# Kernel tuning notes

Measured on AMD Instinct MI355X. Metric: run time of the kernel, lower is better.

## Reference

```python
import jax, jax.numpy as jnp
import numpy as np
from jax import lax

TAU = 2.0
NUM_HEADS = 8
EPS = 1e-5
ALPHA = 4.0  # surrogate sigmoid sharpness

@jax.custom_vjp
def heaviside(x):
    # torch.heaviside(x, 1.0): 1 for x >= 0 (value 1 at x==0), 0 for x < 0
    return (x >= 0).astype(x.dtype)

def _hv_fwd(x):
    return (x >= 0).astype(x.dtype), x

def _hv_bwd(x, g):
    s = jax.nn.sigmoid(x * ALPHA)
    return (g * s * (1.0 - s) * ALPHA,)

heaviside.defvjp(_hv_fwd, _hv_bwd)

def lif(x):
    # Leaky-integrate-fire recurrence over leading time axis. x: [T, ...]
    def step(v, xt):
        v = v + (xt - v) / TAU                 # leakage
        s = heaviside(v - 1.0)                 # fire (v_threshold = 1.0)
        v = (1.0 - lax.stop_gradient(s)) * v   # hard reset (detached spike)
        return v, s
    _, spikes = lax.scan(step, jnp.zeros_like(x[0]), x)
    return spikes

def conv1x1(x, w):
    # x: [T,B,Cin,H,W], w: [Cout,Cin] (1x1 conv, no bias)
    return jnp.einsum('tbchw,dc->tbdhw', x, w)

def bn(x, gamma, beta, mean, var):
    # BatchNorm2d in eval mode (running stats), per-channel over axis 2
    shp = (1, 1, -1, 1, 1)
    inv = gamma.reshape(shp) / jnp.sqrt(var.reshape(shp) + EPS)
    return (x - mean.reshape(shp)) * inv + beta.reshape(shp)

def setup_inputs():
    key = jax.random.key(0)
    ks = jax.random.split(key, 10)
    T, B, C, H, W = 4, 32, 256, 16, 16
    Cv = C  # lamda_ratio = 1

    def w_init(k, o, i):
        return jax.random.normal(k, (o, i), jnp.float32) * (1.0 / np.sqrt(i))

    def bn_params(k, c):
        k1, k2, k3, k4 = jax.random.split(k, 4)
        gamma = jax.random.uniform(k1, (c,), jnp.float32, 0.5, 1.5)
        beta = jax.random.normal(k2, (c,), jnp.float32) * 0.1
        mean = jax.random.normal(k3, (c,), jnp.float32) * 0.1
        var = jax.random.uniform(k4, (c,), jnp.float32, 0.5, 1.5)
        return gamma, beta, mean, var

    x = jax.random.normal(ks[0], (T, B, C, H, W), jnp.float32)
    q_w = w_init(ks[1], C, C)
    k_w = w_init(ks[2], C, C)
    v_w = w_init(ks[3], Cv, C)
    proj_w = w_init(ks[4], C, Cv)
    q_gamma, q_beta, q_mean, q_var = bn_params(ks[5], C)
    k_gamma, k_beta, k_mean, k_var = bn_params(ks[6], C)
    v_gamma, v_beta, v_mean, v_var = bn_params(ks[7], Cv)
    p_gamma, p_beta, p_mean, p_var = bn_params(ks[8], C)
    return {
        'x': x,
        'q_w': q_w, 'q_gamma': q_gamma, 'q_beta': q_beta, 'q_mean': q_mean, 'q_var': q_var,
        'k_w': k_w, 'k_gamma': k_gamma, 'k_beta': k_beta, 'k_mean': k_mean, 'k_var': k_var,
        'v_w': v_w, 'v_gamma': v_gamma, 'v_beta': v_beta, 'v_mean': v_mean, 'v_var': v_var,
        'proj_w': proj_w, 'p_gamma': p_gamma, 'p_beta': p_beta, 'p_mean': p_mean, 'p_var': p_var,
    }

def reference(x, q_w, q_gamma, q_beta, q_mean, q_var,
              k_w, k_gamma, k_beta, k_mean, k_var,
              v_w, v_gamma, v_beta, v_mean, v_var,
              proj_w, p_gamma, p_beta, p_mean, p_var):
    T, B, C, H, W = x.shape
    N = H * W
    Cv = v_w.shape[0]
    hd = C // NUM_HEADS
    hdv = Cv // NUM_HEADS
    scale = (C // NUM_HEADS) ** -0.5

    xs = lif(x)  # head_spike

    q = lif(bn(conv1x1(xs, q_w), q_gamma, q_beta, q_mean, q_var))  # [T,B,C,H,W] binary
    k = lif(bn(conv1x1(xs, k_w), k_gamma, k_beta, k_mean, k_var))
    v = lif(bn(conv1x1(xs, v_w), v_gamma, v_beta, v_mean, v_var))  # [T,B,Cv,H,W]

    # channel c = h*hd + d; flatten spatial -> tokens N, split heads
    q = q.reshape(T, B, NUM_HEADS, hd, N).transpose(0, 1, 2, 4, 3)   # [T,B,h,N,d]
    k = k.reshape(T, B, NUM_HEADS, hd, N).transpose(0, 1, 2, 4, 3)
    v = v.reshape(T, B, NUM_HEADS, hdv, N).transpose(0, 1, 2, 4, 3)  # [T,B,h,N,dv]

    attn = jnp.einsum('tbhnd,tbhmd->tbhnm', q, k)                    # QK^T
    out = jnp.einsum('tbhnm,tbhmd->tbhnd', attn, v) * (scale * 2.0)  # (QK^T)V * 2*scale

    out = out.transpose(0, 1, 2, 4, 3).reshape(T, B, Cv, N)          # [T,B,Cv,N]
    out = lif(out)                                                   # attn_spike
    out = out.reshape(T, B, Cv, H, W)
    out = bn(conv1x1(out, proj_w), p_gamma, p_beta, p_mean, p_var)   # [T,B,C,H,W]
    return out
```

## Files before the change

kernel.cpp:

```cpp
#include <hip/hip_runtime.h>

#define TT 4
#define BB 32
#define CC 256
#define NN 256
#define EPSf 1e-5f
#define MULTf 0.35355339059327373f
#define MARGINf 1e-3f
#define FLAG_CAP 524288u

typedef __attribute__((ext_vector_type(8))) short s16x8;
typedef __attribute__((ext_vector_type(4))) float f32x4;
typedef unsigned char uchar;
typedef unsigned int uint;
typedef unsigned short ushort;

__device__ __forceinline__ ushort f2bf_rn(float f) {
  uint u = __float_as_uint(f);
  u = (u + 0x7FFFu + ((u >> 16) & 1u)) >> 16;
  return (ushort)u;
}
__device__ __forceinline__ float bf2f(ushort b) {
  return __uint_as_float(((uint)b) << 16);
}

__device__ __forceinline__ void gload_lds16(const void* g, void* l) {
  __builtin_amdgcn_global_load_lds(
      (const __attribute__((address_space(1))) uint*)g,
      (__attribute__((address_space(3))) uint*)l, 16, 0, 0);
}

__global__ __launch_bounds__(256) void k_front(
    const float* __restrict__ x, uchar* __restrict__ xsF, uchar* __restrict__ xsP,
    const float* __restrict__ qw, const float* __restrict__ kw,
    const float* __restrict__ vw, const float* __restrict__ pw,
    uchar* __restrict__ wfq, uchar* __restrict__ wfp, uint* __restrict__ flags) {
  const int tid = threadIdx.x;
  const int bid = blockIdx.x;
  if (bid < 1024) {
#pragma clang fp contract(off)
    const int nt = bid & 3;
    const int ks = (bid >> 2) & 7;
    const int b = bid >> 5;
    const int nl = tid & 63;
    const int oct = tid >> 6;
    const int n = nt * 64 + nl;
    const int c0 = ks * 32 + oct * 8;
    const size_t stride = (size_t)BB * CC * NN;
    const float* xb = x + ((size_t)b * CC + c0) * NN + n;

    float v[8];
#pragma unroll
    for (int j = 0; j < 8; ++j) v[j] = 0.f;

#pragma unroll
    for (int t = 0; t < TT; ++t) {
      ushort sp[8];
      uint pm = 0;
#pragma unroll
      for (int j = 0; j < 8; ++j) {
        float xt = xb[t * stride + (size_t)j * NN];
        float d = (xt - v[j]) * 0.5f;
        v[j] = v[j] + d;
        bool s = (v[j] >= 1.0f);
        sp[j] = s ? (ushort)0x3F80 : (ushort)0;
        if (s) { v[j] = 0.f; pm |= 1u << j; }
      }
      uint4* dst = reinterpret_cast<uint4*>(xsF) +
                   (((size_t)(t * BB + b) * 16 + (n >> 4)) * 512 + ks * 64 + oct * 16 + (n & 15));
      uint4 o;
      o.x = (uint)sp[0] | ((uint)sp[1] << 16);
      o.y = (uint)sp[2] | ((uint)sp[3] << 16);
      o.z = (uint)sp[4] | ((uint)sp[5] << 16);
      o.w = (uint)sp[6] | ((uint)sp[7] << 16);
      *dst = o;
      xsP[(((size_t)(t * BB + b) * NN + n) << 5) + ks * 4 + oct] = (uchar)pm;
    }
  } else {
    const int gid = (bid - 1024) * 256 + tid;
    if (gid < 4) flags[gid] = 0;
    const int ob2 = gid >> 9;
    const int e = gid & 511;
    const int ks = e >> 6, l = e & 63;
    const float* W;
    uchar* outb;
    int ob_out, nob;
    if (ob2 < 48) {
      const int sel = ob2 >> 4;
      W = sel == 0 ? qw : (sel == 1 ? kw : vw);
      W += ((size_t)((ob2 & 15) * 16 + (l & 15))) * CC;
      outb = wfq; ob_out = ob2; nob = 48;
    } else {
      W = pw + ((size_t)((ob2 - 48) * 16 + (l & 15))) * CC;
      outb = wfp; ob_out = ob2 - 48; nob = 16;
    }
    const int c0 = ks * 32 + (l >> 4) * 8;
    float wv[8];
    *reinterpret_cast<float4*>(&wv[0]) = *reinterpret_cast<const float4*>(W + c0);
    *reinterpret_cast<float4*>(&wv[4]) = *reinterpret_cast<const float4*>(W + c0 + 4);
    ushort hi[8], lo[8];
#pragma unroll
    for (int j = 0; j < 8; ++j) {
      hi[j] = f2bf_rn(wv[j]);
      lo[j] = f2bf_rn(wv[j] - bf2f(hi[j]));
    }
    const size_t base = (((size_t)ob_out * 8 + ks) * 64 + l) * 16;
    const size_t sstr = (size_t)nob * 8 * 64 * 16;
    *reinterpret_cast<uint4*>(outb + base) = *reinterpret_cast<const uint4*>(hi);
    *reinterpret_cast<uint4*>(outb + sstr + base) = *reinterpret_cast<const uint4*>(lo);
  }
}

__global__ __launch_bounds__(256) void k_qkv_mfma(
    const uchar* __restrict__ xsF, const uchar* __restrict__ wfq,
    const float* __restrict__ qga, const float* __restrict__ qbe, const float* __restrict__ qme, const float* __restrict__ qva,
    const float* __restrict__ kga, const float* __restrict__ kbe, const float* __restrict__ kme, const float* __restrict__ kva,
    const float* __restrict__ vga, const float* __restrict__ vbe, const float* __restrict__ vme, const float* __restrict__ vva,
    ushort* __restrict__ qp, uint* __restrict__ flags) {
  __shared__ short wlds[64][64][8];
  const int tid = threadIdx.x;
  const int w = tid >> 6, lane = tid & 63;
  const int lhi = lane >> 4, llo = lane & 15;
  const int wr = w >> 1, wc = w & 1;
  const int bid = blockIdx.x;
  const int xcd = bid & 7;
  const int r = bid >> 3;
  const int j = r % 12;
  const int g = (r / 12) * 8 + xcd;
  const int b = g >> 2, ntile = g & 3;
  const int oc0 = j * 64;
  const int sel = j >> 2;
  const float* G  = sel == 0 ? qga : (sel == 1 ? kga : vga);
  const float* Be = sel == 0 ? qbe : (sel == 1 ? kbe : vbe);
  const float* Mn = sel == 0 ? qme : (sel == 1 ? kme : vme);
  const float* Vr = sel == 0 ? qva : (sel == 1 ? kva : vva);

#pragma unroll
  for (int i = 0; i < 16; ++i) {
    const int cg = w * 16 + i;
    const int s = cg >> 5, rem = cg & 31, obl = rem >> 3, ks = rem & 7;
    const size_t gsrc = ((((size_t)s * 48 + j * 4 + obl) * 8 + ks) * 64 + lane) * 16;
    gload_lds16(wfq + gsrc, reinterpret_cast<char*>(&wlds[0][0][0]) + cg * 1024);
  }

  float inv8[2][4], mean8[2][4], beta8[2][4];
#pragma unroll
  for (int mf = 0; mf < 2; ++mf)
#pragma unroll
    for (int rr = 0; rr < 4; ++rr) {
      const int ocb = (oc0 & 255) + wr * 32 + mf * 16 + lhi * 4 + rr;
      inv8[mf][rr] = G[ocb] / sqrtf(Vr[ocb] + EPSf);
      mean8[mf][rr] = Mn[ocb];
      beta8[mf][rr] = Be[ocb];
    }

  float vst[2][2][4];
#pragma unroll
  for (int mf = 0; mf < 2; ++mf)
#pragma unroll
    for (int nf = 0; nf < 2; ++nf)
#pragma unroll
      for (int rr = 0; rr < 4; ++rr) vst[mf][nf][rr] = 0.f;
  uint fl = 0;
  ushort qm[TT][4];

  const int nb0 = ntile * 4 + wc * 2;
  __syncthreads();

#define BPTR(t_, nb_, ks_)                                              \
  reinterpret_cast<const s16x8*>(                                       \
      xsF + ((((size_t)((t_) * BB + b) * 16 + (nb_)) * 512 + (ks_) * 64 + lane) * 16))

  s16x8 bA[2][8], bB[2][8];
#pragma unroll
  for (int ks = 0; ks < 8; ++ks) {
    bA[0][ks] = *BPTR(0, nb0, ks);
    bA[1][ks] = *BPTR(0, nb0 + 1, ks);
  }

#define QKV_STEP(t_, CUR, NXT, PRE)                                             \
  {                                                                             \
    if (PRE) {                                                                  \
      _Pragma("unroll") for (int ks = 0; ks < 8; ++ks) {                        \
        NXT[0][ks] = *BPTR((t_) + 1, nb0, ks);                                  \
        NXT[1][ks] = *BPTR((t_) + 1, nb0 + 1, ks);                              \
      }                                                                         \
    }                                                                           \
    f32x4 acc[2][2];                                                            \
    _Pragma("unroll") for (int mf = 0; mf < 2; ++mf)                            \
        _Pragma("unroll") for (int nf = 0; nf < 2; ++nf)                        \
            acc[mf][nf] = (f32x4){0.f, 0.f, 0.f, 0.f};                          \
    _Pragma("unroll") for (int ks = 0; ks < 8; ++ks) {                          \
      _Pragma("unroll") for (int s = 0; s < 2; ++s)                             \
          _Pragma("unroll") for (int mf = 0; mf < 2; ++mf) {                    \
        s16x8 wf = *reinterpret_cast<const s16x8*>(                             \
            &wlds[s * 32 + (wr * 2 + mf) * 8 + ks][lane][0]);                   \
        acc[mf][0] = __builtin_amdgcn_mfma_f32_16x16x32_bf16(wf, CUR[0][ks],    \
                                                             acc[mf][0], 0, 0, 0); \
        acc[mf][1] = __builtin_amdgcn_mfma_f32_16x16x32_bf16(wf, CUR[1][ks],    \
                                                             acc[mf][1], 0, 0, 0); \
      }                                                                         \
    }                                                                           \
    _Pragma("unroll") for (int mf = 0; mf < 2; ++mf)                            \
        _Pragma("unroll") for (int nf = 0; nf < 2; ++nf)                        \
            _Pragma("unroll") for (int rr = 0; rr < 4; ++rr) {                  \
      float y = (acc[mf][nf][rr] - mean8[mf][rr]) * inv8[mf][rr] + beta8[mf][rr]; \
      float v = vst[mf][nf][rr];                                                \
      v = v + (y - v) * 0.5f;                                                   \
      const bool sp = (v >= 1.0f);                                              \
      if (fabsf(v - 1.0f) < MARGINf) fl |= 1u << ((mf * 2 + nf) * 4 + rr);      \
      const unsigned long long m = __ballot(sp);                                \
      if (llo == rr) qm[t_][mf * 2 + nf] = (ushort)((m >> (lhi * 16)) & 0xFFFFull); \
      vst[mf][nf][rr] = sp ? 0.f : v;                                           \
    }                                                                           \
  }

  QKV_STEP(0, bA, bB, 1)
  QKV_STEP(1, bB, bA, 1)
  QKV_STEP(2, bA, bB, 1)
  QKV_STEP(3, bB, bA, 0)
#undef QKV_STEP
#undef BPTR

  if (llo < 4) {
#pragma unroll
    for (int t = 0; t < TT; ++t) {
      ushort* qrow = qp + (size_t)(t * BB + b) * 768 * 16;
#pragma unroll
      for (int mf = 0; mf < 2; ++mf)
#pragma unroll
        for (int nf = 0; nf < 2; ++nf) {
          const int oc = oc0 + wr * 32 + mf * 16 + lhi * 4 + llo;
          qrow[(size_t)oc * 16 + ntile * 4 + wc * 2 + nf] = qm[t][mf * 2 + nf];
        }
    }
  }

  if (fl) {
    const int cnt = __popc(fl);
    uint base = atomicAdd(flags, (uint)cnt);
#pragma unroll
    for (int mf = 0; mf < 2; ++mf)
#pragma unroll
      for (int nf = 0; nf < 2; ++nf)
#pragma unroll
        for (int rr = 0; rr < 4; ++rr)
          if (fl & (1u << ((mf * 2 + nf) * 4 + rr))) {
            const int oc = oc0 + wr * 32 + mf * 16 + lhi * 4 + rr;
            const int n = ntile * 64 + wc * 32 + nf * 16 + llo;
            if (base < FLAG_CAP) flags[4 + base] = (((uint)(b << 10) | (uint)oc) << 8) | (uint)n;
            base++;
          }
  }
}

__global__ __launch_bounds__(256) void k_fix(
    const uchar* __restrict__ xsP,
    const float* __restrict__ qw, const float* __restrict__ kw, const float* __restrict__ vw,
    const float* __restrict__ qga, const float* __restrict__ qbe, const float* __restrict__ qme, const float* __restrict__ qva,
    const float* __restrict__ kga, const float* __restrict__ kbe, const float* __restrict__ kme, const float* __restrict__ kva,
    const float* __restrict__ vga, const float* __restrict__ vbe, const float* __restrict__ vme, const float* __restrict__ vva,
    uint* __restrict__ qp32, const uint* __restrict__ flags) {
#pragma clang fp contract(off)
  const uint cnt = min(flags[0], FLAG_CAP);
  for (uint i = blockIdx.x * 256 + threadIdx.x; i < cnt; i += gridDim.x * 256) {
    const uint e = flags[4 + i];
    const int n = e & 255;
    const int oc = (e >> 8) & 1023;
    const int b = e >> 18;
    const int sel = oc >> 8, ocl = oc & 255;
    const float* W = (sel == 0 ? qw : (sel == 1 ? kw : vw)) + (size_t)ocl * CC;
    const float* G  = sel == 0 ? qga : (sel == 1 ? kga : vga);
    const float* Be = sel == 0 ? qbe : (sel == 1 ? kbe : vbe);
    const float* Mn = sel == 0 ? qme : (sel == 1 ? kme : vme);
    const float* Vr = sel == 0 ? qva : (sel == 1 ? kva : vva);

    uint bw[4][8];
#pragma unroll
    for (int t = 0; t < TT; ++t) {
      const uint4* p = reinterpret_cast<const uint4*>(
          xsP + (((size_t)(t * BB + b) * NN + n) << 5));
      uint4 a = p[0], c4 = p[1];
      bw[t][0] = a.x;  bw[t][1] = a.y;  bw[t][2] = a.z;  bw[t][3] = a.w;
      bw[t][4] = c4.x; bw[t][5] = c4.y; bw[t][6] = c4.z; bw[t][7] = c4.w;
    }

    const float4* W4 = reinterpret_cast<const float4*>(W);
    float a0 = 0.f, a1 = 0.f, a2 = 0.f, a3 = 0.f;
#pragma unroll
    for (int g = 0; g < 32; ++g) {
      const float4 w0 = W4[2 * g];
      const float4 w1 = W4[2 * g + 1];
      const uint s0 = bw[0][g >> 2] >> ((g & 3) * 8);
      const uint s1 = bw[1][g >> 2] >> ((g & 3) * 8);
      const uint s2 = bw[2][g >> 2] >> ((g & 3) * 8);
      const uint s3 = bw[3][g >> 2] >> ((g & 3) * 8);
      const float wv[8] = {w0.x, w0.y, w0.z, w0.w, w1.x, w1.y, w1.z, w1.w};
#pragma unroll
      for (int jj = 0; jj < 8; ++jj) {
        a0 = fmaf(wv[jj], (float)((s0 >> jj) & 1u), a0);
        a1 = fmaf(wv[jj], (float)((s1 >> jj) & 1u), a1);
        a2 = fmaf(wv[jj], (float)((s2 >> jj) & 1u), a2);
        a3 = fmaf(wv[jj], (float)((s3 >> jj) & 1u), a3);
      }
    }
    float accs[4] = {a0, a1, a2, a3};

    const float inv = G[ocl] / sqrtf(Vr[ocl] + EPSf);
    const float mean = Mn[ocl], beta = Be[ocl];
    float v = 0.f;
#pragma unroll
    for (int t = 0; t < TT; ++t) {
      float xm = accs[t] - mean;
      float y = xm * inv;
      y = y + beta;
      float d = (y - v) * 0.5f;
      v = v + d;
      const bool sp = (v >= 1.0f);
      const size_t widx = ((size_t)(t * BB + b) * 768 + oc) * 8 + (n >> 5);
      const uint bit = 1u << (n & 31);
      if (sp) atomicOr(&qp32[widx], bit);
      else atomicAnd(&qp32[widx], ~bit);
      if (sp) v = 0.f;
    }
  }
}

__global__ __launch_bounds__(1024) void k_attn(const ushort* __restrict__ qp,
                                               uchar* __restrict__ attnF) {
  __shared__ uint Qb[32][8], Kb[32][8], Vb[32][8];
  __shared__ int KtV[32][32];
  const int tid = threadIdx.x;
  const int b = blockIdx.x >> 3;
  const int h = blockIdx.x & 7;
  const int n = tid & 255;
  const int jg = tid >> 8;
  const int wordn = n >> 5, bitn = n & 31;

  float vst[8];
#pragma unroll
  for (int j = 0; j < 8; ++j) vst[j] = 0.f;

  for (int t = 0; t < TT; ++t) {
    __syncthreads();
    const ushort* base = qp + (size_t)(t * BB + b) * 768 * 16;
    if (tid < 768) {
      const int arr = tid >> 8;
      const int idx = tid & 255;
      const int ch = idx >> 3, wv2 = idx & 7;
      const uint val = *reinterpret_cast<const uint*>(
          base + (size_t)(arr * 256 + h * 32 + ch) * 16 + wv2 * 2);
      uint(*dst)[8] = (arr == 0) ? Qb : (arr == 1) ? Kb : Vb;
      dst[ch][wv2] = val;
    }
    __syncthreads();
    {
      const int ii = tid >> 5, jj = tid & 31;
      int s = 0;
#pragma unroll
      for (int w8 = 0; w8 < 8; ++w8) s += __popc(Kb[ii][w8] & Vb[jj][w8]);
      KtV[ii][jj] = s;
    }
    __syncthreads();
    int acc[8];
#pragma unroll
    for (int j = 0; j < 8; ++j) acc[j] = 0;
#pragma unroll 4
    for (int ii = 0; ii < 32; ++ii) {
      const int qb = (int)((Qb[ii][wordn] >> bitn) & 1u);
      const int4 k0 = *reinterpret_cast<const int4*>(&KtV[ii][jg * 8]);
      const int4 k1 = *reinterpret_cast<const int4*>(&KtV[ii][jg * 8 + 4]);
      acc[0] += k0.x * qb; acc[1] += k0.y * qb;
      acc[2] += k0.z * qb; acc[3] += k0.w * qb;
      acc[4] += k1.x * qb; acc[5] += k1.y * qb;
      acc[6] += k1.z * qb; acc[7] += k1.w * qb;
    }
    ushort sbit[8];
    {
#pragma clang fp contract(off)
#pragma unroll
      for (int j = 0; j < 8; ++j) {
        float y = (float)acc[j] * MULTf;
        float v = vst[j];
        float d = (y - v) * 0.5f;
        v = v + d;
        const bool sp = (v >= 1.0f);
        sbit[j] = sp ? (ushort)0x3F80 : (ushort)0;
        vst[j] = sp ? 0.f : v;
      }
    }
    uint4 o;
    o.x = (uint)sbit[0] | ((uint)sbit[1] << 16);
    o.y = (uint)sbit[2] | ((uint)sbit[3] << 16);
    o.z = (uint)sbit[4] | ((uint)sbit[5] << 16);
    o.w = (uint)sbit[6] | ((uint)sbit[7] << 16);
    uint4* dst4 = reinterpret_cast<uint4*>(attnF) +
                  (((size_t)(t * BB + b) * 16 + (n >> 4)) * 512 + h * 64 + jg * 16 + (n & 15));
    *dst4 = o;
  }
}

__global__ __launch_bounds__(256) void k_proj_mfma(
    const uchar* __restrict__ attnF, const uchar* __restrict__ wfp,
    const float* __restrict__ pga, const float* __restrict__ pbe,
    const float* __restrict__ pme, const float* __restrict__ pva,
    float* __restrict__ out) {
  const int tid = threadIdx.x;
  const int w = tid >> 6, lane = tid & 63;
  const int lhi = lane >> 4, llo = lane & 15;
  const int wr = w >> 1, wc = w & 1;
  const int bid = blockIdx.x;
  const int xcd = bid & 7;
  const int r = bid >> 3;
  const int j = r & 3;
  const int g = (r >> 2) * 8 + xcd;
  const int tb = g >> 2, ntile = g & 3;
  const int oc0 = j * 64;

  s16x8 wfr[2][2][8];
#pragma unroll
  for (int s = 0; s < 2; ++s)
#pragma unroll
    for (int mf = 0; mf < 2; ++mf) {
      const int ob = j * 4 + wr * 2 + mf;
#pragma unroll
      for (int ks = 0; ks < 8; ++ks)
        wfr[s][mf][ks] = *reinterpret_cast<const s16x8*>(
            wfp + ((((size_t)s * 16 + ob) * 8 + ks) * 64 + lane) * 16);
    }

  const int nb0 = ntile * 4 + wc * 2;
  s16x8 bfr[2][8];
#pragma unroll
  for (int ks = 0; ks < 8; ++ks) {
    bfr[0][ks] = *reinterpret_cast<const s16x8*>(
        attnF + ((((size_t)tb * 16 + nb0) * 512 + ks * 64 + lane) * 16));
    bfr[1][ks] = *reinterpret_cast<const s16x8*>(
        attnF + ((((size_t)tb * 16 + nb0 + 1) * 512 + ks * 64 + lane) * 16));
  }

  float inv8[2][4], mean8[2][4], beta8[2][4];
#pragma unroll
  for (int mf = 0; mf < 2; ++mf)
#pragma unroll
    for (int rr = 0; rr < 4; ++rr) {
      const int ocb = oc0 + wr * 32 + mf * 16 + lhi * 4 + rr;
      inv8[mf][rr] = pga[ocb] / sqrtf(pva[ocb] + EPSf);
      mean8[mf][rr] = pme[ocb];
      beta8[mf][rr] = pbe[ocb];
    }

  f32x4 acc[2][2];
#pragma unroll
  for (int mf = 0; mf < 2; ++mf)
#pragma unroll
    for (int nf = 0; nf < 2; ++nf) acc[mf][nf] = (f32x4){0.f, 0.f, 0.f, 0.f};

#pragma unroll
  for (int ks = 0; ks < 8; ++ks) {
#pragma unroll
    for (int s = 0; s < 2; ++s)
#pragma unroll
      for (int mf = 0; mf < 2; ++mf) {
        acc[mf][0] = __builtin_amdgcn_mfma_f32_16x16x32_bf16(wfr[s][mf][ks], bfr[0][ks], acc[mf][0], 0, 0, 0);
        acc[mf][1] = __builtin_amdgcn_mfma_f32_16x16x32_bf16(wfr[s][mf][ks], bfr[1][ks], acc[mf][1], 0, 0, 0);
      }
  }

#pragma unroll
  for (int mf = 0; mf < 2; ++mf)
#pragma unroll
    for (int nf = 0; nf < 2; ++nf)
#pragma unroll
      for (int rr = 0; rr < 4; ++rr) {
        const int oc = oc0 + wr * 32 + mf * 16 + lhi * 4 + rr;
        const int nn = ntile * 64 + wc * 32 + nf * 16 + llo;
        float y = (acc[mf][nf][rr] - mean8[mf][rr]) * inv8[mf][rr] + beta8[mf][rr];
        out[((size_t)tb * CC + oc) * NN + nn] = y;
      }
}

extern "C" void kernel_launch(void* const* d_in, const int* in_sizes, int n_in,
                              void* d_out, int out_size, void* d_ws, size_t ws_size,
                              hipStream_t stream) {
  const float* x = (const float*)d_in[0];
  const float* q_w = (const float*)d_in[1];
  const float* q_g = (const float*)d_in[2];
  const float* q_b = (const float*)d_in[3];
  const float* q_m = (const float*)d_in[4];
  const float* q_v = (const float*)d_in[5];
  const float* k_w = (const float*)d_in[6];
  const float* k_g = (const float*)d_in[7];
  const float* k_b = (const float*)d_in[8];
  const float* k_m = (const float*)d_in[9];
  const float* k_v = (const float*)d_in[10];
  const float* v_w = (const float*)d_in[11];
  const float* v_g = (const float*)d_in[12];
  const float* v_b = (const float*)d_in[13];
  const float* v_m = (const float*)d_in[14];
  const float* v_v = (const float*)d_in[15];
  const float* p_w = (const float*)d_in[16];
  const float* p_g = (const float*)d_in[17];
  const float* p_b = (const float*)d_in[18];
  const float* p_m = (const float*)d_in[19];
  const float* p_v = (const float*)d_in[20];

  uchar* ws = (uchar*)d_ws;
  uchar* xsF  = ws;
  ushort* qp  = (ushort*)(ws + 16777216);
  uchar* wfq  = ws + 19922944;
  uchar* wfp  = ws + 20709376;
  uint* flags = (uint*)(ws + 20971520);
  uchar* xsP  = ws + 23068672;

  k_front<<<dim3(1152), 256, 0, stream>>>(x, xsF, xsP, q_w, k_w, v_w, p_w,
                                          wfq, wfp, flags);
  k_qkv_mfma<<<dim3(1536), 256, 0, stream>>>(xsF, wfq,
                                             q_g, q_b, q_m, q_v,
                                             k_g, k_b, k_m, k_v,
                                             v_g, v_b, v_m, v_v,
                                             qp, flags);
  k_fix<<<dim3(64), 256, 0, stream>>>(xsP, q_w, k_w, v_w,
                                      q_g, q_b, q_m, q_v,
                                      k_g, k_b, k_m, k_v,
                                      v_g, v_b, v_m, v_v,
                                      (uint*)qp, flags);
  k_attn<<<dim3(256), 1024, 0, stream>>>(qp, xsF );
  k_proj_mfma<<<dim3(2048), 256, 0, stream>>>(xsF, wfp, p_g, p_b, p_m, p_v,
                                              (float*)d_out);
}
```

Before: 112.3 us.

## Fold BN scale into single-bf16 QKV weights and widen fix-up margin

The QKV weights are now pre-scaled by the BN inverse std and stored as a single bf16 (hi only) instead of a hi/lo split. This halves the MFMA count, and the QKV kernel keeps weight fragments in registers instead of LDS, with one wave per 16-column tile. To absorb the larger bf16 error, the near-threshold margin grows tenfold, the flag capacity grows, and the exact fp32 fix-up kernel launches with more blocks. The front kernel also vectorizes the input LIF to four tokens per thread. The trade is fewer MFMAs and less LDS traffic against possibly many more flagged elements to recompute exactly.

New measurement: 111.0 us. No clear change (-1.2%).

```diff
diff --git a/kernel.cpp b/kernel.cpp
--- a/kernel.cpp
+++ b/kernel.cpp
@@ -6,8 +6,8 @@
 #define NN 256
 #define EPSf 1e-5f
 #define MULTf 0.35355339059327373f
-#define MARGINf 1e-3f
-#define FLAG_CAP 524288u
+#define MARGINQ 1e-2f
+#define FLAG_CAP 2097152u
 
 typedef __attribute__((ext_vector_type(8))) short s16x8;
 typedef __attribute__((ext_vector_type(4))) float f32x4;
@@ -24,109 +24,121 @@
   return __uint_as_float(((uint)b) << 16);
 }
 
-__device__ __forceinline__ void gload_lds16(const void* g, void* l) {
-  __builtin_amdgcn_global_load_lds(
-      (const __attribute__((address_space(1))) uint*)g,
-      (__attribute__((address_space(3))) uint*)l, 16, 0, 0);
-}
-
 __global__ __launch_bounds__(256) void k_front(
     const float* __restrict__ x, uchar* __restrict__ xsF, uchar* __restrict__ xsP,
     const float* __restrict__ qw, const float* __restrict__ kw,
     const float* __restrict__ vw, const float* __restrict__ pw,
+    const float* __restrict__ qga, const float* __restrict__ qva,
+    const float* __restrict__ kga, const float* __restrict__ kva,
+    const float* __restrict__ vga, const float* __restrict__ vva,
     uchar* __restrict__ wfq, uchar* __restrict__ wfp, uint* __restrict__ flags) {
   const int tid = threadIdx.x;
   const int bid = blockIdx.x;
-  if (bid < 1024) {
+  if (bid < 256) {
 #pragma clang fp contract(off)
-    const int nt = bid & 3;
-    const int ks = (bid >> 2) & 7;
-    const int b = bid >> 5;
-    const int nl = tid & 63;
+    const int b = bid >> 3;
+    const int ksq = bid & 7;
     const int oct = tid >> 6;
-    const int n = nt * 64 + nl;
-    const int c0 = ks * 32 + oct * 8;
+    const int nq = tid & 63;
+    const int c0 = ksq * 32 + oct * 8;
+    const int n0 = nq * 4;
     const size_t stride = (size_t)BB * CC * NN;
-    const float* xb = x + ((size_t)b * CC + c0) * NN + n;
-
-    float v[8];
-#pragma unroll
-    for (int j = 0; j < 8; ++j) v[j] = 0.f;
+    const float* xb = x + ((size_t)b * CC + c0) * NN + n0;
+
+    float v[8][4];
+#pragma unroll
+    for (int j = 0; j < 8; ++j)
+#pragma unroll
+      for (int nn = 0; nn < 4; ++nn) v[j][nn] = 0.f;
 
 #pragma unroll
     for (int t = 0; t < TT; ++t) {
-      ushort sp[8];
-      uint pm = 0;
+      ushort sp[8][4];
+      uint pm[4] = {0, 0, 0, 0};
 #pragma unroll
       for (int j = 0; j < 8; ++j) {
-        float xt = xb[t * stride + (size_t)j * NN];
-        float d = (xt - v[j]) * 0.5f;
-        v[j] = v[j] + d;
-        bool s = (v[j] >= 1.0f);
-        sp[j] = s ? (ushort)0x3F80 : (ushort)0;
-        if (s) { v[j] = 0.f; pm |= 1u << j; }
-      }
-      uint4* dst = reinterpret_cast<uint4*>(xsF) +
-                   (((size_t)(t * BB + b) * 16 + (n >> 4)) * 512 + ks * 64 + oct * 16 + (n & 15));
-      uint4 o;
-      o.x = (uint)sp[0] | ((uint)sp[1] << 16);
-      o.y = (uint)sp[2] | ((uint)sp[3] << 16);
-      o.z = (uint)sp[4] | ((uint)sp[5] << 16);
-      o.w = (uint)sp[6] | ((uint)sp[7] << 16);
-      *dst = o;
-      xsP[(((size_t)(t * BB + b) * NN + n) << 5) + ks * 4 + oct] = (uchar)pm;
+        const float4 xv = *reinterpret_cast<const float4*>(xb + t * stride + (size_t)j * NN);
+        const float xa[4] = {xv.x, xv.y, xv.z, xv.w};
+#pragma unroll
+        for (int nn = 0; nn < 4; ++nn) {
+          float d = (xa[nn] - v[j][nn]) * 0.5f;
+          v[j][nn] = v[j][nn] + d;
+          bool s = (v[j][nn] >= 1.0f);
+          sp[j][nn] = s ? (ushort)0x3F80 : (ushort)0;
+          if (s) { v[j][nn] = 0.f; pm[nn] |= 1u << j; }
+        }
+      }
+#pragma unroll
+      for (int nn = 0; nn < 4; ++nn) {
+        const int n = n0 + nn;
+        uint4* dst = reinterpret_cast<uint4*>(xsF) +
+                     (((size_t)(t * BB + b) * 16 + (n >> 4)) * 512 + ksq * 64 + oct * 16 + (n & 15));
+        uint4 o;
+        o.x = (uint)sp[0][nn] | ((uint)sp[1][nn] << 16);
+        o.y = (uint)sp[2][nn] | ((uint)sp[3][nn] << 16);
+        o.z = (uint)sp[4][nn] | ((uint)sp[5][nn] << 16);
+        o.w = (uint)sp[6][nn] | ((uint)sp[7][nn] << 16);
+        *dst = o;
+        xsP[(((size_t)(t * BB + b) * NN + n) << 5) + ksq * 4 + oct] = (uchar)pm[nn];
+      }
     }
   } else {
-    const int gid = (bid - 1024) * 256 + tid;
+    const int gid = (bid - 256) * 256 + tid;
     if (gid < 4) flags[gid] = 0;
     const int ob2 = gid >> 9;
     const int e = gid & 511;
     const int ks = e >> 6, l = e & 63;
-    const float* W;
-    uchar* outb;
-    int ob_out, nob;
+    const int c0 = ks * 32 + (l >> 4) * 8;
     if (ob2 < 48) {
       const int sel = ob2 >> 4;
-      W = sel == 0 ? qw : (sel == 1 ? kw : vw);
-      W += ((size_t)((ob2 & 15) * 16 + (l & 15))) * CC;
-      outb = wfq; ob_out = ob2; nob = 48;
+      const float* Wb = sel == 0 ? qw : (sel == 1 ? kw : vw);
+      const float* G = sel == 0 ? qga : (sel == 1 ? kga : vga);
+      const float* Vr = sel == 0 ? qva : (sel == 1 ? kva : vva);
+      const int ocr = (ob2 & 15) * 16 + (l & 15);
+      const float inv = G[ocr] / sqrtf(Vr[ocr] + EPSf);
+      const float* W = Wb + (size_t)ocr * CC;
+      float wv[8];
+      *reinterpret_cast<float4*>(&wv[0]) = *reinterpret_cast<const float4*>(W + c0);
+      *reinterpret_cast<float4*>(&wv[4]) = *reinterpret_cast<const float4*>(W + c0 + 4);
+      ushort hi[8];
+#pragma unroll
+      for (int j = 0; j < 8; ++j) hi[j] = f2bf_rn(wv[j] * inv);
+      *reinterpret_cast<uint4*>(wfq + (((size_t)ob2 * 8 + ks) * 64 + l) * 16) =
+          *reinterpret_cast<const uint4*>(hi);
     } else {
-      W = pw + ((size_t)((ob2 - 48) * 16 + (l & 15))) * CC;
-      outb = wfp; ob_out = ob2 - 48; nob = 16;
-    }
-    const int c0 = ks * 32 + (l >> 4) * 8;
-    float wv[8];
-    *reinterpret_cast<float4*>(&wv[0]) = *reinterpret_cast<const float4*>(W + c0);
-    *reinterpret_cast<float4*>(&wv[4]) = *reinterpret_cast<const float4*>(W + c0 + 4);
-    ushort hi[8], lo[8];
-#pragma unroll
-    for (int j = 0; j < 8; ++j) {
-      hi[j] = f2bf_rn(wv[j]);
-      lo[j] = f2bf_rn(wv[j] - bf2f(hi[j]));
-    }
-    const size_t base = (((size_t)ob_out * 8 + ks) * 64 + l) * 16;
-    const size_t sstr = (size_t)nob * 8 * 64 * 16;
-    *reinterpret_cast<uint4*>(outb + base) = *reinterpret_cast<const uint4*>(hi);
-    *reinterpret_cast<uint4*>(outb + sstr + base) = *reinterpret_cast<const uint4*>(lo);
-  }
-}
-
-__global__ __launch_bounds__(256) void k_qkv_mfma(
+      const int ob = ob2 - 48;
+      const float* W = pw + ((size_t)(ob * 16 + (l & 15))) * CC;
+      float wv[8];
+      *reinterpret_cast<float4*>(&wv[0]) = *reinterpret_cast<const float4*>(W + c0);
+      *reinterpret_cast<float4*>(&wv[4]) = *reinterpret_cast<const float4*>(W + c0 + 4);
+      ushort hi[8], lo[8];
+#pragma unroll
+      for (int j = 0; j < 8; ++j) {
+        hi[j] = f2bf_rn(wv[j]);
+        lo[j] = f2bf_rn(wv[j] - bf2f(hi[j]));
+      }
+      const size_t base = (((size_t)ob * 8 + ks) * 64 + l) * 16;
+      const size_t sstr = (size_t)16 * 8 * 64 * 16;
+      *reinterpret_cast<uint4*>(wfp + base) = *reinterpret_cast<const uint4*>(hi);
+      *reinterpret_cast<uint4*>(wfp + sstr + base) = *reinterpret_cast<const uint4*>(lo);
+    }
+  }
+}
+
+__global__ __launch_bounds__(256, 2) void k_qkv_mfma(
     const uchar* __restrict__ xsF, const uchar* __restrict__ wfq,
     const float* __restrict__ qga, const float* __restrict__ qbe, const float* __restrict__ qme, const float* __restrict__ qva,
     const float* __restrict__ kga, const float* __restrict__ kbe, const float* __restrict__ kme, const float* __restrict__ kva,
     const float* __restrict__ vga, const float* __restrict__ vbe, const float* __restrict__ vme, const float* __restrict__ vva,
     ushort* __restrict__ qp, uint* __restrict__ flags) {
-  __shared__ short wlds[64][64][8];
   const int tid = threadIdx.x;
-  const int w = tid >> 6, lane = tid & 63;
+  const int wc = tid >> 6, lane = tid & 63;
   const int lhi = lane >> 4, llo = lane & 15;
-  const int wr = w >> 1, wc = w & 1;
   const int bid = blockIdx.x;
   const int xcd = bid & 7;
-  const int r = bid >> 3;
-  const int j = r % 12;
-  const int g = (r / 12) * 8 + xcd;
+  const int r0 = bid >> 3;
+  const int j = r0 % 12;
+  const int g = (r0 / 12) * 8 + xcd;
   const int b = g >> 2, ntile = g & 3;
   const int oc0 = j * 64;
   const int sel = j >> 2;
@@ -135,91 +147,70 @@
   const float* Mn = sel == 0 ? qme : (sel == 1 ? kme : vme);
   const float* Vr = sel == 0 ? qva : (sel == 1 ? kva : vva);
 
-#pragma unroll
-  for (int i = 0; i < 16; ++i) {
-    const int cg = w * 16 + i;
-    const int s = cg >> 5, rem = cg & 31, obl = rem >> 3, ks = rem & 7;
-    const size_t gsrc = ((((size_t)s * 48 + j * 4 + obl) * 8 + ks) * 64 + lane) * 16;
-    gload_lds16(wfq + gsrc, reinterpret_cast<char*>(&wlds[0][0][0]) + cg * 1024);
-  }
-
-  float inv8[2][4], mean8[2][4], beta8[2][4];
-#pragma unroll
-  for (int mf = 0; mf < 2; ++mf)
+  s16x8 wfr[4][8];
+#pragma unroll
+  for (int mf = 0; mf < 4; ++mf)
+#pragma unroll
+    for (int ks = 0; ks < 8; ++ks)
+      wfr[mf][ks] = *reinterpret_cast<const s16x8*>(
+          wfq + (((size_t)(j * 4 + mf) * 8 + ks) * 64 + lane) * 16);
+
+  float bias8[4][4];
+#pragma unroll
+  for (int mf = 0; mf < 4; ++mf)
 #pragma unroll
     for (int rr = 0; rr < 4; ++rr) {
-      const int ocb = (oc0 & 255) + wr * 32 + mf * 16 + lhi * 4 + rr;
-      inv8[mf][rr] = G[ocb] / sqrtf(Vr[ocb] + EPSf);
-      mean8[mf][rr] = Mn[ocb];
-      beta8[mf][rr] = Be[ocb];
-    }
-
-  float vst[2][2][4];
-#pragma unroll
-  for (int mf = 0; mf < 2; ++mf)
-#pragma unroll
-    for (int nf = 0; nf < 2; ++nf)
-#pragma unroll
-      for (int rr = 0; rr < 4; ++rr) vst[mf][nf][rr] = 0.f;
+      const int ocb = (j & 3) * 64 + mf * 16 + lhi * 4 + rr;
+      const float inv = G[ocb] / sqrtf(Vr[ocb] + EPSf);
+      bias8[mf][rr] = Be[ocb] - Mn[ocb] * inv;
+    }
+
+  float vst[4][4];
+#pragma unroll
+  for (int mf = 0; mf < 4; ++mf)
+#pragma unroll
+    for (int rr = 0; rr < 4; ++rr) vst[mf][rr] = 0.f;
   uint fl = 0;
   ushort qm[TT][4];
 
-  const int nb0 = ntile * 4 + wc * 2;
-  __syncthreads();
-
-#define BPTR(t_, nb_, ks_)                                              \
+  const int nb = ntile * 4 + wc;
+
+#define BPTR(t_, ks_)                                                   \
   reinterpret_cast<const s16x8*>(                                       \
-      xsF + ((((size_t)((t_) * BB + b) * 16 + (nb_)) * 512 + (ks_) * 64 + lane) * 16))
-
-  s16x8 bA[2][8], bB[2][8];
-#pragma unroll
-  for (int ks = 0; ks < 8; ++ks) {
-    bA[0][ks] = *BPTR(0, nb0, ks);
-    bA[1][ks] = *BPTR(0, nb0 + 1, ks);
-  }
-
-#define QKV_STEP(t_, CUR, NXT, PRE)                                             \
-  {                                                                             \
-    if (PRE) {                                                                  \
-      _Pragma("unroll") for (int ks = 0; ks < 8; ++ks) {                        \
-        NXT[0][ks] = *BPTR((t_) + 1, nb0, ks);                                  \
-        NXT[1][ks] = *BPTR((t_) + 1, nb0 + 1, ks);                              \
-      }                                                                         \
-    }                                                                           \
-    f32x4 acc[2][2];                                                            \
-    _Pragma("unroll") for (int mf = 0; mf < 2; ++mf)                            \
-        _Pragma("unroll") for (int nf = 0; nf < 2; ++nf)                        \
-            acc[mf][nf] = (f32x4){0.f, 0.f, 0.f, 0.f};                          \
-    _Pragma("unroll") for (int ks = 0; ks < 8; ++ks) {                          \
-      _Pragma("unroll") for (int s = 0; s < 2; ++s)                             \
-          _Pragma("unroll") for (int mf = 0; mf < 2; ++mf) {                    \
-        s16x8 wf = *reinterpret_cast<const s16x8*>(                             \
-            &wlds[s * 32 + (wr * 2 + mf) * 8 + ks][lane][0]);                   \
-        acc[mf][0] = __builtin_amdgcn_mfma_f32_16x16x32_bf16(wf, CUR[0][ks],    \
-                                                             acc[mf][0], 0, 0, 0); \
-        acc[mf][1] = __builtin_amdgcn_mfma_f32_16x16x32_bf16(wf, CUR[1][ks],    \
-                                                             acc[mf][1], 0, 0, 0); \
-      }                                                                         \
-    }                                                                           \
-    _Pragma("unroll") for (int mf = 0; mf < 2; ++mf)                            \
-        _Pragma("unroll") for (int nf = 0; nf < 2; ++nf)                        \
-            _Pragma("unroll") for (int rr = 0; rr < 4; ++rr) {                  \
-      float y = (acc[mf][nf][rr] - mean8[mf][rr]) * inv8[mf][rr] + beta8[mf][rr]; \
-      float v = vst[mf][nf][rr];                                                \
-      v = v + (y - v) * 0.5f;                                                   \
-      const bool sp = (v >= 1.0f);                                              \
-      if (fabsf(v - 1.0f) < MARGINf) fl |= 1u << ((mf * 2 + nf) * 4 + rr);      \
-      const unsigned long long m = __ballot(sp);                                \
-      if (llo == rr) qm[t_][mf * 2 + nf] = (ushort)((m >> (lhi * 16)) & 0xFFFFull); \
-      vst[mf][nf][rr] = sp ? 0.f : v;                                           \
-    }                                                                           \
-  }
-
-  QKV_STEP(0, bA, bB, 1)
-  QKV_STEP(1, bB, bA, 1)
-  QKV_STEP(2, bA, bB, 1)
-  QKV_STEP(3, bB, bA, 0)
-#undef QKV_STEP
+      xsF + ((((size_t)((t_) * BB + b) * 16 + nb) * 512 + (ks_) * 64 + lane) * 16))
+
+  s16x8 bfr[8];
+#pragma unroll
+  for (int ks = 0; ks < 8; ++ks) bfr[ks] = *BPTR(0, ks);
+
+#pragma unroll
+  for (int t = 0; t < TT; ++t) {
+    f32x4 acc[4];
+#pragma unroll
+    for (int mf = 0; mf < 4; ++mf) acc[mf] = (f32x4){0.f, 0.f, 0.f, 0.f};
+
+#pragma unroll
+    for (int ks = 0; ks < 8; ++ks) {
+#pragma unroll
+      for (int mf = 0; mf < 4; ++mf)
+        acc[mf] = __builtin_amdgcn_mfma_f32_16x16x32_bf16(wfr[mf][ks], bfr[ks], acc[mf], 0, 0, 0);
+      if (t < TT - 1) bfr[ks] = *BPTR(t + 1, ks);
+    }
+
+#pragma unroll
+    for (int mf = 0; mf < 4; ++mf)
+#pragma unroll
+      for (int rr = 0; rr < 4; ++rr) {
+        float y = acc[mf][rr] + bias8[mf][rr];
+        float v = vst[mf][rr];
+        v = v + (y - v) * 0.5f;
+        const bool sp = (v >= 1.0f);
+        if (fabsf(v - 1.0f) < MARGINQ) fl |= 1u << (mf * 4 + rr);
+        const unsigned long long m = __ballot(sp);
+        if (llo == rr) qm[t][mf] = (ushort)((m >> (lhi * 16)) & 0xFFFFull);
+        vst[mf][rr] = sp ? 0.f : v;
+      }
+  }
 #undef BPTR
 
   if (llo < 4) {
@@ -227,12 +218,10 @@
     for (int t = 0; t < TT; ++t) {
       ushort* qrow = qp + (size_t)(t * BB + b) * 768 * 16;
 #pragma unroll
-      for (int mf = 0; mf < 2; ++mf)
-#pragma unroll
-        for (int nf = 0; nf < 2; ++nf) {
-          const int oc = oc0 + wr * 32 + mf * 16 + lhi * 4 + llo;
-          qrow[(size_t)oc * 16 + ntile * 4 + wc * 2 + nf] = qm[t][mf * 2 + nf];
-        }
+      for (int mf = 0; mf < 4; ++mf) {
+        const int oc = oc0 + mf * 16 + lhi * 4 + llo;
+        qrow[(size_t)oc * 16 + ntile * 4 + wc] = qm[t][mf];
+      }
     }
   }
 
@@ -240,17 +229,15 @@
     const int cnt = __popc(fl);
     uint base = atomicAdd(flags, (uint)cnt);
 #pragma unroll
-    for (int mf = 0; mf < 2; ++mf)
-#pragma unroll
-      for (int nf = 0; nf < 2; ++nf)
-#pragma unroll
-        for (int rr = 0; rr < 4; ++rr)
-          if (fl & (1u << ((mf * 2 + nf) * 4 + rr))) {
-            const int oc = oc0 + wr * 32 + mf * 16 + lhi * 4 + rr;
-            const int n = ntile * 64 + wc * 32 + nf * 16 + llo;
-            if (base < FLAG_CAP) flags[4 + base] = (((uint)(b << 10) | (uint)oc) << 8) | (uint)n;
-            base++;
-          }
+    for (int mf = 0; mf < 4; ++mf)
+#pragma unroll
+      for (int rr = 0; rr < 4; ++rr)
+        if (fl & (1u << (mf * 4 + rr))) {
+          const int oc = oc0 + mf * 16 + lhi * 4 + rr;
+          const int n = ntile * 64 + wc * 16 + llo;
+          if (base < FLAG_CAP) flags[4 + base] = (((uint)(b << 10) | (uint)oc) << 8) | (uint)n;
+          base++;
+        }
   }
 }
 
@@ -288,13 +275,13 @@
     const float4* W4 = reinterpret_cast<const float4*>(W);
     float a0 = 0.f, a1 = 0.f, a2 = 0.f, a3 = 0.f;
 #pragma unroll
-    for (int g = 0; g < 32; ++g) {
-      const float4 w0 = W4[2 * g];
-      const float4 w1 = W4[2 * g + 1];
-      const uint s0 = bw[0][g >> 2] >> ((g & 3) * 8);
-      const uint s1 = bw[1][g >> 2] >> ((g & 3) * 8);
-      const uint s2 = bw[2][g >> 2] >> ((g & 3) * 8);
-      const uint s3 = bw[3][g >> 2] >> ((g & 3) * 8);
+    for (int gg = 0; gg < 32; ++gg) {
+      const float4 w0 = W4[2 * gg];
+      const float4 w1 = W4[2 * gg + 1];
+      const uint s0 = bw[0][gg >> 2] >> ((gg & 3) * 8);
+      const uint s1 = bw[1][gg >> 2] >> ((gg & 3) * 8);
+      const uint s2 = bw[2][gg >> 2] >> ((gg & 3) * 8);
+      const uint s3 = bw[3][gg >> 2] >> ((gg & 3) * 8);
       const float wv[8] = {w0.x, w0.y, w0.z, w0.w, w1.x, w1.y, w1.z, w1.w};
 #pragma unroll
       for (int jj = 0; jj < 8; ++jj) {
@@ -509,22 +496,23 @@
   uchar* xsF  = ws;
   ushort* qp  = (ushort*)(ws + 16777216);
   uchar* wfq  = ws + 19922944;
-  uchar* wfp  = ws + 20709376;
-  uint* flags = (uint*)(ws + 20971520);
-  uchar* xsP  = ws + 23068672;
-
-  k_front<<<dim3(1152), 256, 0, stream>>>(x, xsF, xsP, q_w, k_w, v_w, p_w,
-                                          wfq, wfp, flags);
+  uchar* wfp  = ws + 20447232;
+  uchar* xsP  = ws + 20971520;
+  uint* flags = (uint*)(ws + 22020096);
+
+  k_front<<<dim3(384), 256, 0, stream>>>(x, xsF, xsP, q_w, k_w, v_w, p_w,
+                                         q_g, q_v, k_g, k_v, v_g, v_v,
+                                         wfq, wfp, flags);
   k_qkv_mfma<<<dim3(1536), 256, 0, stream>>>(xsF, wfq,
                                              q_g, q_b, q_m, q_v,
                                              k_g, k_b, k_m, k_v,
                                              v_g, v_b, v_m, v_v,
                                              qp, flags);
-  k_fix<<<dim3(64), 256, 0, stream>>>(xsP, q_w, k_w, v_w,
-                                      q_g, q_b, q_m, q_v,
-                                      k_g, k_b, k_m, k_v,
-                                      v_g, v_b, v_m, v_v,
-                                      (uint*)qp, flags);
+  k_fix<<<dim3(768), 256, 0, stream>>>(xsP, q_w, k_w, v_w,
+                                       q_g, q_b, q_m, q_v,
+                                       k_g, k_b, k_m, k_v,
+                                       v_g, v_b, v_m, v_v,
+                                       (uint*)qp, flags);
   k_attn<<<dim3(256), 1024, 0, stream>>>(qp, xsF );
   k_proj_mfma<<<dim3(2048), 256, 0, stream>>>(xsF, wfp, p_g, p_b, p_m, p_v,
                                               (float*)d_out);
```
